# Kernel optimization log

Measured on AMD Instinct MI355X. Metric: run time of the kernel, lower is better.

The kernel has to match this reference:

```python
import jax, jax.numpy as jnp
import numpy as np

T_STEPS, N, STATE, HID, ACT, C = 32, 64, 64, 128, 32, 96


def setup_inputs() -> dict:
    key = jax.random.key(0)
    ks = jax.random.split(key, 16)
    s = 0.05
    inp = {
        'x': jax.random.normal(ks[0], (T_STEPS, N, STATE), jnp.float32),
        'a': jax.random.normal(ks[1], (T_STEPS, N, ACT), jnp.float32),
        # GRU layer 0 (input state_dim) and layer 1 (input hidden_dim)
        'wih0': jax.random.normal(ks[2], (3 * HID, STATE), jnp.float32) * s,
        'whh0': jax.random.normal(ks[3], (3 * HID, HID), jnp.float32) * s,
        'bih0': jax.random.normal(ks[4], (3 * HID,), jnp.float32) * s,
        'bhh0': jax.random.normal(ks[5], (3 * HID,), jnp.float32) * s,
        'wih1': jax.random.normal(ks[6], (3 * HID, HID), jnp.float32) * s,
        'whh1': jax.random.normal(ks[7], (3 * HID, HID), jnp.float32) * s,
        'bih1': jax.random.normal(ks[8], (3 * HID,), jnp.float32) * s,
        'bhh1': jax.random.normal(ks[9], (3 * HID,), jnp.float32) * s,
        'w1': jax.random.normal(ks[10], (HID, HID + ACT), jnp.float32) * s,
        'b1': jax.random.normal(ks[11], (HID,), jnp.float32) * s,
        'w2': jax.random.normal(ks[12], (1, 2 * HID), jnp.float32) * s,
        'b2': jax.random.normal(ks[13], (1,), jnp.float32) * s,
        'Tm': jax.random.normal(ks[14], (HID, HID, C), jnp.float32),  # init.normal(T,0,1)
    }
    return inp


def _gru_cell(x_t, h, wih, whh, bih, bhh):
    gi = x_t @ wih.T + bih            # (N, 3H)
    gh = h @ whh.T + bhh
    i_r, i_z, i_n = jnp.split(gi, 3, axis=-1)
    h_r, h_z, h_n = jnp.split(gh, 3, axis=-1)
    r = jax.nn.sigmoid(i_r + h_r)
    z = jax.nn.sigmoid(i_z + h_z)
    n = jnp.tanh(i_n + r * h_n)
    return (1.0 - z) * n + z * h


def reference(x, a, wih0, whh0, bih0, bhh0, wih1, whh1, bih1, bhh1, w1, b1, w2, b2, Tm):
    def step(h, x_t):
        h0 = _gru_cell(x_t, h[0], wih0, whh0, bih0, bhh0)
        h1 = _gru_cell(h0, h[1], wih1, whh1, bih1, bhh1)
        return jnp.stack([h0, h1]), h1

    h_init = jnp.zeros((2, N, HID), x.dtype)
    _, p = jax.lax.scan(step, h_init, x)              # (T, N, H)

    fc1 = jax.nn.relu(jnp.concatenate([p, a], -1) @ w1.T + b1)  # (T, N, H)

    Tflat = Tm.reshape(HID, HID * C)

    def batch_discrim(xt):  # xt: (N, H)
        M = (xt @ Tflat).reshape(N, HID, C)           # (N, B, C)
        # pairwise L1 over C: (N, N, B)
        norm = jnp.abs(M[:, None] - M[None, :]).sum(-1)
        o_b = (jnp.exp(-norm).sum(0) - 1.0) / (N - 1)  # (N, B)
        return jnp.concatenate([xt, o_b], 1)          # (N, 2H)

    fc2 = jax.lax.map(batch_discrim, fc1)             # (T, N, 2H)
    prob = jax.nn.sigmoid(fc2 @ w2.T + b2)            # (T, N, 1)
    return prob
```

## Files before the change

### kernel.cpp

```cpp
#include <hip/hip_runtime.h>
#include <hip/hip_fp16.h>
#include <cstdint>

#define T_STEPS 32
#define NB 64
#define STATE 64
#define HID 128
#define ACT 32
#define CDIM 96
#define G3 (3*HID)

typedef __attribute__((ext_vector_type(8))) short short8;
typedef __attribute__((ext_vector_type(4))) float f32x4;
typedef _Float16 h2v __attribute__((ext_vector_type(2)));

__device__ __forceinline__ unsigned short f2bf(float f){
  unsigned int u = __builtin_bit_cast(unsigned int, f);
  u = u + 0x7FFFu + ((u >> 16) & 1u);
  return (unsigned short)(u >> 16);
}
__device__ __forceinline__ float bf2f(unsigned short u){
  unsigned int v = ((unsigned int)u) << 16; return __builtin_bit_cast(float, v);
}
__device__ __forceinline__ unsigned int packh2(float f0, float f1){
  return (unsigned int)__half_as_ushort(__float2half_rn(f0)) |
         ((unsigned int)__half_as_ushort(__float2half_rn(f1)) << 16);
}
__device__ __forceinline__ float sigmoidf_(float x){ return 1.0f/(1.0f + __expf(-x)); }
__device__ __forceinline__ float tanhf_(float x){ float e = __expf(2.0f*x); return (e-1.0f)/(e+1.0f); }

__device__ __forceinline__ float dot2f(float acc, unsigned int a, unsigned int b){
  h2v av = __builtin_bit_cast(h2v, a);
  h2v bv = __builtin_bit_cast(h2v, b);
  return __builtin_amdgcn_fdot2(av, bv, acc, false);
}
__device__ __forceinline__ float l1d(float acc, unsigned int ua, unsigned int ub){
  __half2 a = __builtin_bit_cast(__half2, ua);
  __half2 b = __builtin_bit_cast(__half2, ub);
  __half2 d = __habs2(__hsub2(a, b));
  h2v dv = __builtin_bit_cast(h2v, d);
  h2v ones; ones[0] = (_Float16)1.0f; ones[1] = (_Float16)1.0f;
  return __builtin_amdgcn_fdot2(dv, ones, acc, false);
}
__device__ __forceinline__ float l1d4(float acc, uint4 a, uint4 b){
  acc = l1d(acc, a.x, b.x); acc = l1d(acc, a.y, b.y);
  acc = l1d(acc, a.z, b.z); acc = l1d(acc, a.w, b.w);
  return acc;
}

__global__ void k_prep(const float* __restrict__ Tm, unsigned short* __restrict__ tmh,
                       const float* __restrict__ whh0, const float* __restrict__ whh1,
                       const float* __restrict__ w1, const float* __restrict__ wih0,
                       const float* __restrict__ wih1, const float* __restrict__ a,
                       unsigned int* __restrict__ whh0p, unsigned int* __restrict__ whh1p,
                       unsigned short* __restrict__ w1f, unsigned int* __restrict__ wih0p,
                       unsigned int* __restrict__ wih1p, unsigned short* __restrict__ h1af){
  int tid = threadIdx.x;
  int bx = blockIdx.x;
  if (bx < 128){
    int b = bx;
    for (int e = tid; e < HID*CDIM; e += 256){
      int chunk = e / 768;
      int r1 = e - chunk*768;
      int c = r1 >> 3, h = r1 & 7;
      int k = chunk*8 + h;
      tmh[b*(HID*CDIM) + e] = f2bf(Tm[k*(HID*CDIM) + b*CDIM + c]);
    }
  } else if (bx < 132){
    for (int e = (bx-128)*256 + tid; e < 24576; e += 1024){
      int k2 = e / 384, r = e - k2*384;
      whh0p[e] = packh2(whh0[r*128 + 2*k2], whh0[r*128 + 2*k2 + 1]);
      whh1p[e] = packh2(whh1[r*128 + 2*k2], whh1[r*128 + 2*k2 + 1]);
    }
  } else if (bx < 136){
    for (int e = (bx-132)*256 + tid; e < 20480; e += 1024){
      int kc = e >> 10, rem = e & 1023;
      int col = rem >> 3, j = rem & 7;
      w1f[e] = f2bf(w1[col*160 + kc*8 + j]);
    }
  } else if (bx < 138){
    for (int e = (bx-136)*256 + tid; e < 12288; e += 512){
      int k2 = e / 384, r = e - k2*384;
      wih0p[e] = packh2(wih0[r*64 + 2*k2], wih0[r*64 + 2*k2 + 1]);
    }
  } else if (bx < 142){
    for (int e = (bx-138)*256 + tid; e < 24576; e += 1024){
      int k2 = e / 384, r = e - k2*384;
      wih1p[e] = packh2(wih1[r*128 + 2*k2], wih1[r*128 + 2*k2 + 1]);
    }
  } else {
    for (int e = (bx-142)*256 + tid; e < 65536; e += 3072){
      int t = e >> 11, rem = e & 2047;
      int n = rem >> 5, c = rem & 31;
      int pos = t*10240 + (n>>4)*2560 + (16 + (c>>3))*128 + (n&15)*8 + (c&7);
      h1af[pos] = f2bf(a[t*(NB*ACT) + n*ACT + c]);
    }
  }
}

__global__ __launch_bounds__(768, 3) void k_rec0(const float* __restrict__ x,
                                                 const unsigned int* __restrict__ wihp,
                                                 const unsigned int* __restrict__ whhp,
                                                 const float* __restrict__ bih, const float* __restrict__ bhh,
                                                 unsigned short* __restrict__ h0g){
  __shared__ __align__(16) unsigned int xall[1024];
  __shared__ __align__(16) unsigned int hl[64];
  __shared__ float A0[G3];
  __shared__ float GI[2][G3];
  int n = blockIdx.x, tid = threadIdx.x;
  int r = tid >> 1, kh = tid & 1;
  unsigned int wh[32], wi[16];
  #pragma unroll
  for (int i = 0; i < 32; i++) wh[i] = whhp[(kh*32 + i)*384 + r];
  #pragma unroll
  for (int i = 0; i < 16; i++) wi[i] = wihp[(kh*16 + i)*384 + r];
  float bh = (kh == 0) ? bhh[r] : 0.0f;
  float bi = (kh == 0) ? bih[r] : 0.0f;
  for (int e = tid; e < 1024; e += 768){
    int t_ = e >> 5, i = e & 31;
    const float* xp = x + t_*(NB*STATE) + n*STATE + 2*i;
    xall[e] = packh2(xp[0], xp[1]);
  }
  if (tid < 64) hl[tid] = 0u;
  float hprev = 0.0f;
  __syncthreads();
  const uint4* xl4 = (const uint4*)xall;
  const uint4* h4  = (const uint4*)hl;
  {
    float gi = bi;
    #pragma unroll
    for (int j = 0; j < 4; j++){
      uint4 xv = xl4[kh*4 + j];
      gi = dot2f(gi, wi[j*4 + 0], xv.x);
      gi = dot2f(gi, wi[j*4 + 1], xv.y);
      gi = dot2f(gi, wi[j*4 + 2], xv.z);
      gi = dot2f(gi, wi[j*4 + 3], xv.w);
    }
    gi += __shfl_xor(gi, 1);
    if (kh == 0) GI[0][r] = gi;
  }
  __syncthreads();
  for (int t = 0; t < T_STEPS; t++){
    float gh = bh, gin = bi;
    #pragma unroll
    for (int g = 0; g < 2; g++){
      uint4 hv[4];
      #pragma unroll
      for (int j = 0; j < 4; j++) hv[j] = h4[kh*8 + g*4 + j];
      #pragma unroll
      for (int j = 0; j < 4; j++){
        gh = dot2f(gh, wh[g*16 + j*4 + 0], hv[j].x);
        gh = dot2f(gh, wh[g*16 + j*4 + 1], hv[j].y);
        gh = dot2f(gh, wh[g*16 + j*4 + 2], hv[j].z);
        gh = dot2f(gh, wh[g*16 + j*4 + 3], hv[j].w);
      }
    }
    if (t + 1 < T_STEPS){
      #pragma unroll
      for (int j = 0; j < 4; j++){
        uint4 xv = xl4[(t+1)*8 + kh*4 + j];
        gin = dot2f(gin, wi[j*4 + 0], xv.x);
        gin = dot2f(gin, wi[j*4 + 1], xv.y);
        gin = dot2f(gin, wi[j*4 + 2], xv.z);
        gin = dot2f(gin, wi[j*4 + 3], xv.w);
      }
    }
    gh  += __shfl_xor(gh, 1);
    gin += __shfl_xor(gin, 1);
    if (kh == 0){
      A0[r] = gh;
      if (t + 1 < T_STEPS) GI[(t+1)&1][r] = gin;
    }
    __syncthreads();
    if (tid < HID){
      const float* gi = GI[t&1];
      float rg = sigmoidf_(gi[tid]       + A0[tid]);
      float z  = sigmoidf_(gi[tid+HID]   + A0[tid+HID]);
      float nn = tanhf_   (gi[tid+2*HID] + rg*A0[tid+2*HID]);
      float hn = (1.0f - z)*nn + z*hprev;
      hprev = hn;
      ((__half*)hl)[tid] = __float2half_rn(hn);
      h0g[n*4096 + t*128 + tid] = __half_as_ushort(__float2half_rn(hn));
    }
    __syncthreads();
  }
}

__global__ __launch_bounds__(768, 3) void k_rec1(const unsigned short* __restrict__ h0g,
                                                 const unsigned int* __restrict__ wihp,
                                                 const unsigned int* __restrict__ whhp,
                                                 const float* __restrict__ bih, const float* __restrict__ bhh,
                                                 unsigned short* __restrict__ h1af){
  __shared__ __align__(16) unsigned int h0all[2048];
  __shared__ __align__(16) unsigned int hl[64];
  __shared__ float A0[G3];
  __shared__ float GI[2][G3];
  int n = blockIdx.x, tid = threadIdx.x;
  int r = tid >> 1, kh = tid & 1;
  unsigned int wh[32], wi[32];
  #pragma unroll
  for (int i = 0; i < 32; i++) wh[i] = whhp[(kh*32 + i)*384 + r];
  #pragma unroll
  for (int i = 0; i < 32; i++) wi[i] = wihp[(kh*32 + i)*384 + r];
  float bh = (kh == 0) ? bhh[r] : 0.0f;
  float bi = (kh == 0) ? bih[r] : 0.0f;
  const unsigned int* h0u = (const unsigned int*)h0g;
  for (int e = tid; e < 2048; e += 768) h0all[e] = h0u[n*2048 + e];
  if (tid < 64) hl[tid] = 0u;
  float hprev = 0.0f;
  __syncthreads();
  const uint4* h0l4 = (const uint4*)h0all;
  const uint4* h4   = (const uint4*)hl;
  {
    float gi = bi;
    #pragma unroll
    for (int g = 0; g < 2; g++){
      #pragma unroll
      for (int j = 0; j < 4; j++){
        uint4 hv = h0l4[kh*8 + g*4 + j];
        gi = dot2f(gi, wi[g*16 + j*4 + 0], hv.x);
        gi = dot2f(gi, wi[g*16 + j*4 + 1], hv.y);
        gi = dot2f(gi, wi[g*16 + j*4 + 2], hv.z);
        gi = dot2f(gi, wi[g*16 + j*4 + 3], hv.w);
      }
    }
    gi += __shfl_xor(gi, 1);
    if (kh == 0) GI[0][r] = gi;
  }
  __syncthreads();
  for (int t = 0; t < T_STEPS; t++){
    float gh = bh, gin = bi;
    #pragma unroll
    for (int g = 0; g < 2; g++){
      uint4 hv[4];
      #pragma unroll
      for (int j = 0; j < 4; j++) hv[j] = h4[kh*8 + g*4 + j];
      #pragma unroll
      for (int j = 0; j < 4; j++){
        gh = dot2f(gh, wh[g*16 + j*4 + 0], hv[j].x);
        gh = dot2f(gh, wh[g*16 + j*4 + 1], hv[j].y);
        gh = dot2f(gh, wh[g*16 + j*4 + 2], hv[j].z);
        gh = dot2f(gh, wh[g*16 + j*4 + 3], hv[j].w);
      }
    }
    if (t + 1 < T_STEPS){
      #pragma unroll
      for (int g = 0; g < 2; g++){
        #pragma unroll
        for (int j = 0; j < 4; j++){
          uint4 hv = h0l4[(t+1)*16 + kh*8 + g*4 + j];
          gin = dot2f(gin, wi[g*16 + j*4 + 0], hv.x);
          gin = dot2f(gin, wi[g*16 + j*4 + 1], hv.y);
          gin = dot2f(gin, wi[g*16 + j*4 + 2], hv.z);
          gin = dot2f(gin, wi[g*16 + j*4 + 3], hv.w);
        }
      }
    }
    gh  += __shfl_xor(gh, 1);
    gin += __shfl_xor(gin, 1);
    if (kh == 0){
      A0[r] = gh;
      if (t + 1 < T_STEPS) GI[(t+1)&1][r] = gin;
    }
    __syncthreads();
    if (tid < HID){
      const float* gi = GI[t&1];
      float rg = sigmoidf_(gi[tid]       + A0[tid]);
      float z  = sigmoidf_(gi[tid+HID]   + A0[tid+HID]);
      float nn = tanhf_   (gi[tid+2*HID] + rg*A0[tid+2*HID]);
      float hn = (1.0f - z)*nn + z*hprev;
      hprev = hn;
      ((__half*)hl)[tid] = __float2half_rn(hn);
      h1af[t*10240 + (n>>4)*2560 + (tid>>3)*128 + (n&15)*8 + (tid&7)] = f2bf(hn);
    }
    __syncthreads();
  }
}

__global__ __launch_bounds__(256) void k_fc1(const unsigned short* __restrict__ h1af,
                                             const unsigned short* __restrict__ w1f,
                                             const float* __restrict__ b1,
                                             unsigned short* __restrict__ fc1h){
  __shared__ float b1s[128];
  int t = blockIdx.x, tid = threadIdx.x;
  int wave = tid >> 6, lane = tid & 63, m = lane & 15, quad = lane >> 4;
  if (tid < 128) b1s[tid] = b1[tid];
  const uint4* A4 = (const uint4*)(h1af + t*10240);
  const uint4* B4 = (const uint4*)w1f;
  f32x4 acc[8];
  #pragma unroll
  for (int i = 0; i < 8; i++) acc[i] = (f32x4)(0.0f);
  #pragma unroll
  for (int ks = 0; ks < 5; ks++){
    uint4 av = A4[wave*320 + (ks*4 + quad)*16 + m];
    short8 avs = __builtin_bit_cast(short8, av);
    #pragma unroll
    for (int nt = 0; nt < 8; nt++){
      uint4 bv = B4[(ks*4 + quad)*128 + nt*16 + m];
      acc[nt] = __builtin_amdgcn_mfma_f32_16x16x32_bf16(avs, __builtin_bit_cast(short8, bv), acc[nt], 0, 0, 0);
    }
  }
  __syncthreads();
  #pragma unroll
  for (int nt = 0; nt < 8; nt++){
    float bj = b1s[nt*16 + m];
    #pragma unroll
    for (int rr = 0; rr < 4; rr++){
      float v = fmaxf(acc[nt][rr] + bj, 0.0f);
      fc1h[t*8192 + wave*2048 + (nt*2 + (m>>3))*128 + (quad*4 + rr)*8 + (m&7)] = f2bf(v);
    }
  }
}

__global__ __launch_bounds__(256) void k_disc(const unsigned short* __restrict__ fc1h,
                                              const unsigned short* __restrict__ tmh,
                                              float* __restrict__ O){
  __shared__ __align__(16) __half Mh[2][64*104];
  __shared__ float ps[2][64*18];
  int b = blockIdx.x;
  int tid = threadIdx.x;
  int wave = tid >> 6, lane = tid & 63, m = lane & 15, quad = lane >> 4;
  int t0 = blockIdx.y*4;
  const uint4* Bg = (const uint4*)(tmh + b*(CDIM*HID));
  uint4 a4[4];
  #pragma unroll
  for (int kk = 0; kk < 4; kk++) a4[kk] = ((const uint4*)(fc1h + t0*8192))[wave*256 + (kk*4 + quad)*16 + m];
  #pragma unroll 1
  for (int tt = 0; tt < 4; tt++){
    int p = tt & 1;
    int t = t0 + tt;
    f32x4 acc[6];
    #pragma unroll
    for (int i = 0; i < 6; i++) acc[i] = (f32x4)(0.0f);
    #pragma unroll
    for (int kk = 0; kk < 4; kk++){
      short8 av = __builtin_bit_cast(short8, a4[kk]);
      #pragma unroll
      for (int nt = 0; nt < 6; nt++){
        uint4 b4 = Bg[(kk*4 + quad)*96 + nt*16 + m];
        acc[nt] = __builtin_amdgcn_mfma_f32_16x16x32_bf16(av, __builtin_bit_cast(short8, b4), acc[nt], 0, 0, 0);
      }
    }
    if (tt < 3){
      #pragma unroll
      for (int kk = 0; kk < 4; kk++) a4[kk] = ((const uint4*)(fc1h + (t+1)*8192))[wave*256 + (kk*4 + quad)*16 + m];
    }
    #pragma unroll
    for (int nt = 0; nt < 6; nt++){
      #pragma unroll
      for (int rr = 0; rr < 4; rr++){
        Mh[p][(rr*16 + wave*4 + quad)*104 + nt*16 + m] = __float2half(acc[nt][rr]);
      }
    }
    __syncthreads();
    if (tt > 0 && tid < NB){
      float s = 0.0f;
      #pragma unroll
      for (int k = 0; k < 16; k++) s += ps[1-p][tid*18 + k];
      O[((t-1)*HID + b)*NB + tid] = s*(1.0f/63.0f);
    }
    const uint4* M4 = (const uint4*)Mh[p];
    if (tid < 240){
      int chalf = tid & 1, tp = tid >> 1;
      int rnd = tp >> 3, slot = tp & 7;
      int ta, tb;
      if (slot == 0){ ta = 15; tb = rnd; }
      else {
        ta = rnd + slot;      if (ta >= 15) ta -= 15;
        tb = rnd + 15 - slot; if (tb >= 15) tb -= 15;
      }
      float facc[16];
      #pragma unroll
      for (int pp = 0; pp < 16; pp++) facc[pp] = 0.0f;
      auto doChunk = [&](int c){
        int ch = chalf*6 + c;
        uint4 av[4], bv[4];
        #pragma unroll
        for (int s = 0; s < 4; s++){
          av[s] = M4[(s*16 + ta)*13 + ch];
          bv[s] = M4[(s*16 + tb)*13 + ch];
        }
        #pragma unroll
        for (int i = 0; i < 4; i++)
          #pragma unroll
          for (int j = 0; j < 4; j++)
            facc[i*4+j] = l1d4(facc[i*4+j], av[i], bv[j]);
      };
      doChunk(0); doChunk(1);
      bool big1 = true;
      #pragma unroll
      for (int pp = 0; pp < 16; pp++) big1 = big1 && (facc[pp] > 14.0f);
      if (!big1){
        doChunk(2); doChunk(3);
        bool big2 = true;
        #pragma unroll
        for (int pp = 0; pp < 16; pp++) big2 = big2 && (facc[pp] > 14.0f);
        if (!big2){ doChunk(4); doChunk(5); }
      }
      float tot[16];
      #pragma unroll
      for (int pp = 0; pp < 16; pp++) tot[pp] = facc[pp] + __shfl_xor(facc[pp], 1);
      if (chalf == 0){
        #pragma unroll
        for (int i = 0; i < 4; i++){
          float s = 0.0f;
          #pragma unroll
          for (int j = 0; j < 4; j++) s += __expf(-tot[i*4+j]);
          ps[p][(ta*4 + i)*18 + tb] = s;
        }
      } else {
        #pragma unroll
        for (int j = 0; j < 4; j++){
          float s = 0.0f;
          #pragma unroll
          for (int i = 0; i < 4; i++) s += __expf(-tot[i*4+j]);
          ps[p][(tb*4 + j)*18 + ta] = s;
        }
      }
    } else {
      int ta = tid - 240;
      float f6[6];
      #pragma unroll
      for (int pp = 0; pp < 6; pp++) f6[pp] = 0.0f;
      auto doChunkS = [&](int ch){
        uint4 rv[4];
        #pragma unroll
        for (int s = 0; s < 4; s++) rv[s] = M4[(s*16 + ta)*13 + ch];
        f6[0] = l1d4(f6[0], rv[0], rv[1]);
        f6[1] = l1d4(f6[1], rv[0], rv[2]);
        f6[2] = l1d4(f6[2], rv[0], rv[3]);
        f6[3] = l1d4(f6[3], rv[1], rv[2]);
        f6[4] = l1d4(f6[4], rv[1], rv[3]);
        f6[5] = l1d4(f6[5], rv[2], rv[3]);
      };
      doChunkS(0); doChunkS(1); doChunkS(2);
      bool big1 = true;
      #pragma unroll
      for (int pp = 0; pp < 6; pp++) big1 = big1 && (f6[pp] > 14.0f);
      if (!big1){
        doChunkS(3); doChunkS(4); doChunkS(5);
        bool big2 = true;
        #pragma unroll
        for (int pp = 0; pp < 6; pp++) big2 = big2 && (f6[pp] > 14.0f);
        if (!big2){
          doChunkS(6); doChunkS(7); doChunkS(8);
          doChunkS(9); doChunkS(10); doChunkS(11);
        }
      }
      float e01 = __expf(-f6[0]), e02 = __expf(-f6[1]), e03 = __expf(-f6[2]);
      float e12 = __expf(-f6[3]), e13 = __expf(-f6[4]), e23 = __expf(-f6[5]);
      ps[p][(ta*4 + 0)*18 + ta] = e01 + e02 + e03;
      ps[p][(ta*4 + 1)*18 + ta] = e01 + e12 + e13;
      ps[p][(ta*4 + 2)*18 + ta] = e02 + e12 + e23;
      ps[p][(ta*4 + 3)*18 + ta] = e03 + e13 + e23;
    }
  }
  __syncthreads();
  if (tid < NB){
    float s = 0.0f;
    #pragma unroll
    for (int k = 0; k < 16; k++) s += ps[1][tid*18 + k];
    O[((t0+3)*HID + b)*NB + tid] = s*(1.0f/63.0f);
  }
}

__global__ __launch_bounds__(256) void k_final(const unsigned short* __restrict__ fc1h,
                                               const float* __restrict__ O,
                                               const float* __restrict__ w2, const float* __restrict__ b2,
                                               float* __restrict__ out){
  __shared__ float ol[NB*HID];
  __shared__ unsigned short fr[8192];
  __shared__ float wl[2*HID + 2];
  int t = blockIdx.x, tid = threadIdx.x;
  for (int i = tid; i < NB*HID; i += 256) ol[i] = O[t*NB*HID + i];
  const uint4* Fg = (const uint4*)(fc1h + t*8192);
  for (int i = tid; i < 1024; i += 256) ((uint4*)fr)[i] = Fg[i];
  if (tid < 2*HID) wl[tid] = w2[tid];
  if (tid == 0) wl[2*HID] = b2[0];
  __syncthreads();
  if (tid < NB){
    float acc = wl[2*HID];
    int base = (tid>>4)*2048 + (tid&15)*8;
    #pragma unroll 8
    for (int j = 0; j < HID; j++) acc += bf2f(fr[base + (j>>3)*128 + (j&7)])*wl[j];
    #pragma unroll 8
    for (int b = 0; b < HID; b++) acc += ol[b*NB + tid]*wl[HID + b];
    out[t*NB + tid] = sigmoidf_(acc);
  }
}

extern "C" void kernel_launch(void* const* d_in, const int* in_sizes, int n_in,
                              void* d_out, int out_size, void* d_ws, size_t ws_size,
                              hipStream_t stream){
  const float* x    = (const float*)d_in[0];
  const float* a    = (const float*)d_in[1];
  const float* wih0 = (const float*)d_in[2];
  const float* whh0 = (const float*)d_in[3];
  const float* bih0 = (const float*)d_in[4];
  const float* bhh0 = (const float*)d_in[5];
  const float* wih1 = (const float*)d_in[6];
  const float* whh1 = (const float*)d_in[7];
  const float* bih1 = (const float*)d_in[8];
  const float* bhh1 = (const float*)d_in[9];
  const float* w1   = (const float*)d_in[10];
  const float* b1   = (const float*)d_in[11];
  const float* w2   = (const float*)d_in[12];
  const float* b2   = (const float*)d_in[13];
  const float* Tm   = (const float*)d_in[14];
  float* ws = (float*)d_ws;
  float* Ows = ws;
  unsigned int* whh0p = (unsigned int*)(ws + 262144);
  unsigned int* whh1p = (unsigned int*)(ws + 286720);
  unsigned int* wih0p = (unsigned int*)(ws + 311296);
  unsigned int* wih1p = (unsigned int*)(ws + 323584);
  unsigned short* tmh  = (unsigned short*)(ws + 348160);
  unsigned short* fc1h = (unsigned short*)(ws + 1134592);
  unsigned short* h1af = (unsigned short*)(ws + 1265664);
  unsigned short* w1f  = (unsigned short*)(ws + 1429504);
  unsigned short* h0g  = (unsigned short*)(ws + 1439744);
  float* out = (float*)d_out;

  k_prep<<<dim3(154), dim3(256), 0, stream>>>(Tm, tmh, whh0, whh1, w1, wih0, wih1, a,
                                              whh0p, whh1p, w1f, wih0p, wih1p, h1af);
  k_rec0<<<dim3(NB), dim3(768), 0, stream>>>(x, wih0p, whh0p, bih0, bhh0, h0g);
  k_rec1<<<dim3(NB), dim3(768), 0, stream>>>(h0g, wih1p, whh1p, bih1, bhh1, h1af);
  k_fc1<<<dim3(T_STEPS), dim3(256), 0, stream>>>(h1af, w1f, b1, fc1h);
  k_disc<<<dim3(HID, T_STEPS/4), dim3(256), 0, stream>>>(fc1h, tmh, Ows);
  k_final<<<dim3(T_STEPS), dim3(256), 0, stream>>>(fc1h, Ows, w2, b2, out);
}
```

Baseline: 210.3 us.

## Prefetch recurrence inputs from global, split prep blocks, finer early-exit in discriminator

The x-to-fp16 packing moves into the prep kernel, and the Tm transpose is split across twice as many blocks. The recurrent kernels stop staging all time steps in shared memory and instead load the next step's inputs from global memory into registers at the top of each step. This is meant to remove the serial staging at kernel start and overlap loads with the hidden-state dot products. The pairwise L1 loops in the discriminator check the exp-underflow threshold after smaller chunks, so more work can be skipped, at the cost of extra branch checks and possible divergence.

```diff
diff --git a/kernel.cpp b/kernel.cpp
--- a/kernel.cpp
+++ b/kernel.cpp
@@ -52,58 +52,66 @@
                        const float* __restrict__ whh0, const float* __restrict__ whh1,
                        const float* __restrict__ w1, const float* __restrict__ wih0,
                        const float* __restrict__ wih1, const float* __restrict__ a,
+                       const float* __restrict__ x,
                        unsigned int* __restrict__ whh0p, unsigned int* __restrict__ whh1p,
                        unsigned short* __restrict__ w1f, unsigned int* __restrict__ wih0p,
-                       unsigned int* __restrict__ wih1p, unsigned short* __restrict__ h1af){
+                       unsigned int* __restrict__ wih1p, unsigned short* __restrict__ h1af,
+                       unsigned int* __restrict__ xp16){
   int tid = threadIdx.x;
   int bx = blockIdx.x;
-  if (bx < 128){
-    int b = bx;
-    for (int e = tid; e < HID*CDIM; e += 256){
+  if (bx < 256){
+    int b = bx >> 1, half = bx & 1;
+    for (int e = half*6144 + tid; e < (half+1)*6144; e += 256){
       int chunk = e / 768;
       int r1 = e - chunk*768;
       int c = r1 >> 3, h = r1 & 7;
       int k = chunk*8 + h;
       tmh[b*(HID*CDIM) + e] = f2bf(Tm[k*(HID*CDIM) + b*CDIM + c]);
     }
-  } else if (bx < 132){
-    for (int e = (bx-128)*256 + tid; e < 24576; e += 1024){
+  } else if (bx < 260){
+    for (int e = (bx-256)*256 + tid; e < 24576; e += 1024){
       int k2 = e / 384, r = e - k2*384;
       whh0p[e] = packh2(whh0[r*128 + 2*k2], whh0[r*128 + 2*k2 + 1]);
       whh1p[e] = packh2(whh1[r*128 + 2*k2], whh1[r*128 + 2*k2 + 1]);
     }
-  } else if (bx < 136){
-    for (int e = (bx-132)*256 + tid; e < 20480; e += 1024){
+  } else if (bx < 264){
+    for (int e = (bx-260)*256 + tid; e < 20480; e += 1024){
       int kc = e >> 10, rem = e & 1023;
       int col = rem >> 3, j = rem & 7;
       w1f[e] = f2bf(w1[col*160 + kc*8 + j]);
     }
-  } else if (bx < 138){
-    for (int e = (bx-136)*256 + tid; e < 12288; e += 512){
+  } else if (bx < 266){
+    for (int e = (bx-264)*256 + tid; e < 12288; e += 512){
       int k2 = e / 384, r = e - k2*384;
       wih0p[e] = packh2(wih0[r*64 + 2*k2], wih0[r*64 + 2*k2 + 1]);
     }
-  } else if (bx < 142){
-    for (int e = (bx-138)*256 + tid; e < 24576; e += 1024){
+  } else if (bx < 270){
+    for (int e = (bx-266)*256 + tid; e < 24576; e += 1024){
       int k2 = e / 384, r = e - k2*384;
       wih1p[e] = packh2(wih1[r*128 + 2*k2], wih1[r*128 + 2*k2 + 1]);
     }
-  } else {
-    for (int e = (bx-142)*256 + tid; e < 65536; e += 3072){
+  } else if (bx < 282){
+    for (int e = (bx-270)*256 + tid; e < 65536; e += 3072){
       int t = e >> 11, rem = e & 2047;
       int n = rem >> 5, c = rem & 31;
       int pos = t*10240 + (n>>4)*2560 + (16 + (c>>3))*128 + (n&15)*8 + (c&7);
       h1af[pos] = f2bf(a[t*(NB*ACT) + n*ACT + c]);
     }
-  }
-}
-
-__global__ __launch_bounds__(768, 3) void k_rec0(const float* __restrict__ x,
+  } else {
+    for (int e = (bx-282)*256 + tid; e < 65536; e += 2048){
+      int n = e >> 10, rem = e & 1023;
+      int t = rem >> 5, j = rem & 31;
+      const float* xp = x + t*(NB*STATE) + n*STATE + 2*j;
+      xp16[e] = packh2(xp[0], xp[1]);
+    }
+  }
+}
+
+__global__ __launch_bounds__(768, 3) void k_rec0(const unsigned int* __restrict__ xp16,
                                                  const unsigned int* __restrict__ wihp,
                                                  const unsigned int* __restrict__ whhp,
                                                  const float* __restrict__ bih, const float* __restrict__ bhh,
                                                  unsigned short* __restrict__ h0g){
-  __shared__ __align__(16) unsigned int xall[1024];
   __shared__ __align__(16) unsigned int hl[64];
   __shared__ float A0[G3];
   __shared__ float GI[2][G3];
@@ -116,21 +124,16 @@
   for (int i = 0; i < 16; i++) wi[i] = wihp[(kh*16 + i)*384 + r];
   float bh = (kh == 0) ? bhh[r] : 0.0f;
   float bi = (kh == 0) ? bih[r] : 0.0f;
-  for (int e = tid; e < 1024; e += 768){
-    int t_ = e >> 5, i = e & 31;
-    const float* xp = x + t_*(NB*STATE) + n*STATE + 2*i;
-    xall[e] = packh2(xp[0], xp[1]);
-  }
   if (tid < 64) hl[tid] = 0u;
   float hprev = 0.0f;
   __syncthreads();
-  const uint4* xl4 = (const uint4*)xall;
-  const uint4* h4  = (const uint4*)hl;
+  const uint4* xg = (const uint4*)(xp16 + n*1024);
+  const uint4* h4 = (const uint4*)hl;
   {
     float gi = bi;
     #pragma unroll
     for (int j = 0; j < 4; j++){
-      uint4 xv = xl4[kh*4 + j];
+      uint4 xv = xg[kh*4 + j];
       gi = dot2f(gi, wi[j*4 + 0], xv.x);
       gi = dot2f(gi, wi[j*4 + 1], xv.y);
       gi = dot2f(gi, wi[j*4 + 2], xv.z);
@@ -141,6 +144,11 @@
   }
   __syncthreads();
   for (int t = 0; t < T_STEPS; t++){
+    uint4 xv[4];
+    if (t + 1 < T_STEPS){
+      #pragma unroll
+      for (int j = 0; j < 4; j++) xv[j] = xg[(t+1)*8 + kh*4 + j];
+    }
     float gh = bh, gin = bi;
     #pragma unroll
     for (int g = 0; g < 2; g++){
@@ -158,11 +166,10 @@
     if (t + 1 < T_STEPS){
       #pragma unroll
       for (int j = 0; j < 4; j++){
-        uint4 xv = xl4[(t+1)*8 + kh*4 + j];
-        gin = dot2f(gin, wi[j*4 + 0], xv.x);
-        gin = dot2f(gin, wi[j*4 + 1], xv.y);
-        gin = dot2f(gin, wi[j*4 + 2], xv.z);
-        gin = dot2f(gin, wi[j*4 + 3], xv.w);
+        gin = dot2f(gin, wi[j*4 + 0], xv[j].x);
+        gin = dot2f(gin, wi[j*4 + 1], xv[j].y);
+        gin = dot2f(gin, wi[j*4 + 2], xv[j].z);
+        gin = dot2f(gin, wi[j*4 + 3], xv[j].w);
       }
     }
     gh  += __shfl_xor(gh, 1);
@@ -191,7 +198,6 @@
                                                  const unsigned int* __restrict__ whhp,
                                                  const float* __restrict__ bih, const float* __restrict__ bhh,
                                                  unsigned short* __restrict__ h1af){
-  __shared__ __align__(16) unsigned int h0all[2048];
   __shared__ __align__(16) unsigned int hl[64];
   __shared__ float A0[G3];
   __shared__ float GI[2][G3];
@@ -204,12 +210,10 @@
   for (int i = 0; i < 32; i++) wi[i] = wihp[(kh*32 + i)*384 + r];
   float bh = (kh == 0) ? bhh[r] : 0.0f;
   float bi = (kh == 0) ? bih[r] : 0.0f;
-  const unsigned int* h0u = (const unsigned int*)h0g;
-  for (int e = tid; e < 2048; e += 768) h0all[e] = h0u[n*2048 + e];
   if (tid < 64) hl[tid] = 0u;
   float hprev = 0.0f;
   __syncthreads();
-  const uint4* h0l4 = (const uint4*)h0all;
+  const uint4* h0gv = (const uint4*)h0g;
   const uint4* h4   = (const uint4*)hl;
   {
     float gi = bi;
@@ -217,7 +221,7 @@
     for (int g = 0; g < 2; g++){
       #pragma unroll
       for (int j = 0; j < 4; j++){
-        uint4 hv = h0l4[kh*8 + g*4 + j];
+        uint4 hv = h0gv[n*512 + kh*8 + g*4 + j];
         gi = dot2f(gi, wi[g*16 + j*4 + 0], hv.x);
         gi = dot2f(gi, wi[g*16 + j*4 + 1], hv.y);
         gi = dot2f(gi, wi[g*16 + j*4 + 2], hv.z);
@@ -229,6 +233,11 @@
   }
   __syncthreads();
   for (int t = 0; t < T_STEPS; t++){
+    uint4 pv[8];
+    if (t + 1 < T_STEPS){
+      #pragma unroll
+      for (int j = 0; j < 8; j++) pv[j] = h0gv[n*512 + (t+1)*16 + kh*8 + j];
+    }
     float gh = bh, gin = bi;
     #pragma unroll
     for (int g = 0; g < 2; g++){
@@ -248,7 +257,7 @@
       for (int g = 0; g < 2; g++){
         #pragma unroll
         for (int j = 0; j < 4; j++){
-          uint4 hv = h0l4[(t+1)*16 + kh*8 + g*4 + j];
+          uint4 hv = pv[g*4 + j];
           gin = dot2f(gin, wi[g*16 + j*4 + 0], hv.x);
           gin = dot2f(gin, wi[g*16 + j*4 + 1], hv.y);
           gin = dot2f(gin, wi[g*16 + j*4 + 2], hv.z);
@@ -386,16 +395,19 @@
           for (int j = 0; j < 4; j++)
             facc[i*4+j] = l1d4(facc[i*4+j], av[i], bv[j]);
       };
-      doChunk(0); doChunk(1);
-      bool big1 = true;
-      #pragma unroll
-      for (int pp = 0; pp < 16; pp++) big1 = big1 && (facc[pp] > 14.0f);
-      if (!big1){
-        doChunk(2); doChunk(3);
-        bool big2 = true;
-        #pragma unroll
-        for (int pp = 0; pp < 16; pp++) big2 = big2 && (facc[pp] > 14.0f);
-        if (!big2){ doChunk(4); doChunk(5); }
+      auto allBig = [&](){
+        bool big = true;
+        #pragma unroll
+        for (int pp = 0; pp < 16; pp++) big = big && (facc[pp] > 14.0f);
+        return big;
+      };
+      doChunk(0);
+      if (!allBig()){
+        doChunk(1);
+        if (!allBig()){
+          doChunk(2); doChunk(3);
+          if (!allBig()){ doChunk(4); doChunk(5); }
+        }
       }
       float tot[16];
       #pragma unroll
@@ -433,18 +445,18 @@
         f6[4] = l1d4(f6[4], rv[1], rv[3]);
         f6[5] = l1d4(f6[5], rv[2], rv[3]);
       };
-      doChunkS(0); doChunkS(1); doChunkS(2);
-      bool big1 = true;
-      #pragma unroll
-      for (int pp = 0; pp < 6; pp++) big1 = big1 && (f6[pp] > 14.0f);
-      if (!big1){
-        doChunkS(3); doChunkS(4); doChunkS(5);
-        bool big2 = true;
-        #pragma unroll
-        for (int pp = 0; pp < 6; pp++) big2 = big2 && (f6[pp] > 14.0f);
-        if (!big2){
-          doChunkS(6); doChunkS(7); doChunkS(8);
-          doChunkS(9); doChunkS(10); doChunkS(11);
+      auto allBigS = [&](){
+        bool big = true;
+        #pragma unroll
+        for (int pp = 0; pp < 6; pp++) big = big && (f6[pp] > 14.0f);
+        return big;
+      };
+      doChunkS(0); doChunkS(1);
+      if (!allBigS()){
+        doChunkS(2); doChunkS(3);
+        if (!allBigS()){
+          doChunkS(4); doChunkS(5); doChunkS(6); doChunkS(7);
+          doChunkS(8); doChunkS(9); doChunkS(10); doChunkS(11);
         }
       }
       float e01 = __expf(-f6[0]), e02 = __expf(-f6[1]), e03 = __expf(-f6[2]);
@@ -518,11 +530,12 @@
   unsigned short* h1af = (unsigned short*)(ws + 1265664);
   unsigned short* w1f  = (unsigned short*)(ws + 1429504);
   unsigned short* h0g  = (unsigned short*)(ws + 1439744);
+  unsigned int* xp16   = (unsigned int*)(ws + 1570816);
   float* out = (float*)d_out;
 
-  k_prep<<<dim3(154), dim3(256), 0, stream>>>(Tm, tmh, whh0, whh1, w1, wih0, wih1, a,
-                                              whh0p, whh1p, w1f, wih0p, wih1p, h1af);
-  k_rec0<<<dim3(NB), dim3(768), 0, stream>>>(x, wih0p, whh0p, bih0, bhh0, h0g);
+  k_prep<<<dim3(290), dim3(256), 0, stream>>>(Tm, tmh, whh0, whh1, w1, wih0, wih1, a, x,
+                                              whh0p, whh1p, w1f, wih0p, wih1p, h1af, xp16);
+  k_rec0<<<dim3(NB), dim3(768), 0, stream>>>(xp16, wih0p, whh0p, bih0, bhh0, h0g);
   k_rec1<<<dim3(NB), dim3(768), 0, stream>>>(h0g, wih1p, whh1p, bih1, bhh1, h1af);
   k_fc1<<<dim3(T_STEPS), dim3(256), 0, stream>>>(h1af, w1f, b1, fc1h);
   k_disc<<<dim3(HID, T_STEPS/4), dim3(256), 0, stream>>>(fc1h, tmh, Ows);
```

Measured after the change: 253.6 us. 1.21x slower.
